# Kernel tuning notes

Measured on AMD Instinct MI355X. Metric: run time of the kernel, lower is better.

Reference implementation:

```python
import jax, jax.numpy as jnp
import numpy as np

B, C, H, W = 8, 64, 64, 64
CI = 32  # inter_channels = in_channels // 2
EPS = 1e-5


def conv1x1(x, w, b=None):
    # x: (b,c,h,w), w: (o,c) -> (b,o,h,w)
    y = jnp.einsum('bchw,oc->bohw', x, w)
    if b is not None:
        y = y + b[None, :, None, None]
    return y


def maxpool2x2(x):
    b, c, h, w = x.shape
    return x.reshape(b, c, h // 2, 2, w // 2, 2).max(axis=(3, 5))


def setup_inputs() -> dict:
    key = jax.random.key(0)
    ks = jax.random.split(key, 12)
    s = 0.05
    return {
        'x': jax.random.normal(ks[0], (B, C, H, W), jnp.float32),
        'theta_w': jax.random.normal(ks[1], (CI, C), jnp.float32) * s,
        'theta_b': jax.random.normal(ks[2], (CI,), jnp.float32) * s,
        'phi_w': jax.random.normal(ks[3], (CI, C), jnp.float32) * s,
        'phi_b': jax.random.normal(ks[4], (CI,), jnp.float32) * s,
        'psi_w': jax.random.normal(ks[5], (CI, C), jnp.float32) * s,
        'psi_b': jax.random.normal(ks[6], (CI,), jnp.float32) * s,
        'cp_w': jax.random.normal(ks[7], (2 * CI,), jnp.float32) * s,  # concat_project 1x1, no bias
        'W_w': jax.random.normal(ks[8], (C, CI + 1), jnp.float32) * s,
        'W_b': jax.random.normal(ks[9], (C,), jnp.float32) * s,
        'bn_gamma': jax.random.normal(ks[10], (C,), jnp.float32) * s + 1.0,
        'bn_beta': jax.random.normal(ks[11], (C,), jnp.float32) * s,
    }


def reference(x, theta_w, theta_b, phi_w, phi_b, psi_w, psi_b, cp_w, W_w, W_b, bn_gamma, bn_beta):
    b = x.shape[0]
    # psi / phi branches get 2x2 maxpool (sub_sample=True default)
    psi_x = maxpool2x2(conv1x1(x, psi_w, psi_b)).reshape(b, CI, -1)      # (b,ci,M)
    psi_x = psi_x.transpose(0, 2, 1)                                     # (b,M,ci)
    theta_x = conv1x1(x, theta_w, theta_b).reshape(b, CI, -1)            # (b,ci,N)
    phi_x = maxpool2x2(conv1x1(x, phi_w, phi_b)).reshape(b, CI, -1)      # (b,ci,M)
    # concat_project(cat[theta_i, phi_j]) + ReLU == relu(w1.theta_i + w2.phi_j)
    w1, w2 = cp_w[:CI], cp_w[CI:]
    a = jnp.einsum('bcn,c->bn', theta_x, w1)                             # (b,N)
    bb = jnp.einsum('bcm,c->bm', phi_x, w2)                              # (b,M)
    f = jax.nn.relu(a[:, :, None] + bb[:, None, :])                      # (b,N,M)
    M = f.shape[-1]
    f_div_C = f / float(M)
    y = jnp.matmul(f_div_C, psi_x)                                       # (b,N,ci)
    y = y.transpose(0, 2, 1).reshape(b, CI, H, W)
    # r_structure_type='zero' -> zero structure channel
    structure_feat = jnp.zeros((b, 1, H, W), y.dtype)
    y = jnp.concatenate([y, structure_feat], axis=1)                     # (b,ci+1,H,W)
    wy = conv1x1(y, W_w, W_b)                                            # (b,C,H,W)
    # BatchNorm2d, training-mode batch stats, biased variance
    mu = wy.mean(axis=(0, 2, 3), keepdims=True)
    var = wy.var(axis=(0, 2, 3), keepdims=True)
    wy = (wy - mu) * jax.lax.rsqrt(var + EPS)
    wy = wy * bn_gamma[None, :, None, None] + bn_beta[None, :, None, None]
    return wy + x
```

## Files before the change

kernel.cpp:

```cpp
#include <hip/hip_runtime.h>

#define OFF_A    0
#define OFF_BB   32768
#define OFF_RK   40960
#define OFF_U    57344
#define OFF_T1   581632
#define OFF_T2   1106432
#define OFF_KK   1631232
#define OFF_MP1  1664000
#define OFF_MP2  1664512
#define OFF_HC   1665024
#define OFF_HS   1673224
#define OFF_HS2  1681424
#define OFF_BAR  1689624

__device__ __forceinline__ void stg(float* p, float v) {
    __hip_atomic_store(p, v, __ATOMIC_RELAXED, __HIP_MEMORY_SCOPE_AGENT);
}
__device__ __forceinline__ float ldg1(const float* p) {
    return __hip_atomic_load(p, __ATOMIC_RELAXED, __HIP_MEMORY_SCOPE_AGENT);
}
__device__ __forceinline__ void stgi(int* p, int v) {
    __hip_atomic_store(p, v, __ATOMIC_RELAXED, __HIP_MEMORY_SCOPE_AGENT);
}
__device__ __forceinline__ int ldgi(const int* p) {
    return __hip_atomic_load(p, __ATOMIC_RELAXED, __HIP_MEMORY_SCOPE_AGENT);
}
__device__ __forceinline__ void stgu(unsigned* p, unsigned v) {
    __hip_atomic_store(p, v, __ATOMIC_RELAXED, __HIP_MEMORY_SCOPE_AGENT);
}
__device__ __forceinline__ unsigned ldgu(const unsigned* p) {
    return __hip_atomic_load(p, __ATOMIC_RELAXED, __HIP_MEMORY_SCOPE_AGENT);
}

__device__ __forceinline__ void gbarBatch(float* ws, int b, unsigned goal)
{
    __syncthreads();
    if (threadIdx.x == 0) {
        unsigned* ctr = (unsigned*)(ws + OFF_BAR) + ((b + 1) << 5);
        __hip_atomic_fetch_add(ctr, 1u, __ATOMIC_RELAXED,
                               __HIP_MEMORY_SCOPE_AGENT);
        while (ldgu(ctr) < goal) __builtin_amdgcn_s_sleep(2);
    }
    __syncthreads();
}

__global__ __launch_bounds__(1024) void kA(
    const float* __restrict__ x, const float* __restrict__ theta_w,
    const float* __restrict__ theta_b, const float* __restrict__ phi_w,
    const float* __restrict__ phi_b, const float* __restrict__ psi_w,
    const float* __restrict__ psi_b, const float* __restrict__ cp_w,
    const float* __restrict__ Ww, float* __restrict__ ws)
{
    __shared__ float sh[7396];
    const int tid = threadIdx.x;
    const int bid = blockIdx.x;
    const int b   = bid >> 5;
    const int sub = bid & 31;
    unsigned* bars = (unsigned*)(ws + OFF_BAR);

    {
        if (bid == 0 && tid == 0) {
            for (int i = 0; i < 8; ++i) stgu(&bars[(i + 1) << 5], 0u);
        }
        if (tid < 97) {
            int e = sub*97 + tid;
            if (e < 1025)      stg(&ws[OFF_HC  + b*1025 + e], 0.0f);
            else if (e < 2050) stg(&ws[OFF_HS  + b*1025 + e - 1025], 0.0f);
            else if (e < 3075) stg(&ws[OFF_HS2 + b*1025 + e - 2050], 0.0f);
        }
        float* sm   = sh;
        float* sth  = sh + 4160;
        float* spsi = sh + 4228;
        float* sWw  = sh + 5284;
        for (int e = tid; e < 2048; e += 1024) {
            int i = e >> 6, c = e & 63;
            sm[i*130 + 2*c]     = phi_w[e];
            sm[i*130 + 2*c + 1] = psi_w[e];
        }
        for (int e = tid; e < 2048; e += 1024)
            sWw[(e >> 5)*33 + (e & 31)] = Ww[(e >> 5)*33 + (e & 31)];
        if (tid < 64) {
            float s = 0;
            for (int i = 0; i < 32; ++i) s += cp_w[i]*theta_w[i*64 + tid];
            sth[tid] = s;
        } else if (tid == 64) {
            float s = 0;
            for (int i = 0; i < 32; ++i) s += cp_w[i]*theta_b[i];
            sth[64] = s;
        }
        __syncthreads();
        if (bid == 0 && tid == 0) {
            stgu(&bars[288], 0x5A5A5A5Au);
            stgu(&bars[289], 0xA5A5A5A5u);
        }
        int i = tid & 31;
        int mIdx = tid >> 5;
        int m = (sub << 5) + mIdx;
        int ph = m >> 5, pw = m & 31;
        const float* xb = x + b*262144 + ph*128 + pw*2;
        const float2* wrow = (const float2*)(sm + i*130);
        float tb = sth[64];
        float p0=0,p1=0,p2=0,p3=0,s0=0,s1=0,s2=0,s3=0;
        float a0=tb,a1=tb,a2=tb,a3=tb;
        #pragma unroll 8
        for (int c = 0; c < 64; ++c) {
            float2 xa = *(const float2*)(xb + c*4096);
            float2 xc = *(const float2*)(xb + c*4096 + 64);
            float2 w  = wrow[c];
            float st  = sth[c];
            p0 += xa.x*w.x; p1 += xa.y*w.x; p2 += xc.x*w.x; p3 += xc.y*w.x;
            s0 += xa.x*w.y; s1 += xa.y*w.y; s2 += xc.x*w.y; s3 += xc.y*w.y;
            a0 += xa.x*st;  a1 += xa.y*st;  a2 += xc.x*st;  a3 += xc.y*st;
        }
        float pv = fmaxf(fmaxf(p0,p1), fmaxf(p2,p3)) + phi_b[i];
        float sv = fmaxf(fmaxf(s0,s1), fmaxf(s2,s3)) + psi_b[i];
        spsi[mIdx*33 + i] = sv;
        float v = pv * cp_w[32 + i];
        v += __shfl_xor(v, 16, 32);
        v += __shfl_xor(v,  8, 32);
        v += __shfl_xor(v,  4, 32);
        v += __shfl_xor(v,  2, 32);
        v += __shfl_xor(v,  1, 32);
        if (i == 0) {
            stg(&ws[OFF_BB + (b<<10) + m], v);
            int nb = (b<<12) + ph*128 + pw*2;
            stg(&ws[OFF_A + nb],      a0);
            stg(&ws[OFF_A + nb + 1],  a1);
            stg(&ws[OFF_A + nb + 64], a2);
            stg(&ws[OFF_A + nb + 65], a3);
        }
        __syncthreads();
        #pragma unroll
        for (int rep = 0; rep < 2; ++rep) {
            int o  = (tid >> 5) + (rep << 5);
            int ml = tid & 31;
            const float* pr = &spsi[ml*33];
            const float* wr = &sWw[o*33];
            float u = 0;
            #pragma unroll
            for (int i2 = 0; i2 < 32; ++i2) u += pr[i2]*wr[i2];
            stg(&ws[OFF_U + (((b<<6) + o)<<10) + (sub<<5) + ml], u);
        }
    }
    __syncthreads();
    if (tid == 0) {
        while ((ldgu(&bars[288]) ^ ldgu(&bars[289])) != 0xFFFFFFFFu)
            __builtin_amdgcn_s_sleep(2);
        unsigned* ctr = bars + ((b + 1) << 5);
        __hip_atomic_fetch_add(ctr, 1u, __ATOMIC_RELAXED,
                               __HIP_MEMORY_SCOPE_AGENT);
        while (ldgu(ctr) < 32u) __builtin_amdgcn_s_sleep(2);
    }
    __syncthreads();

    {
        float* sb = sh;
        sb[tid] = ldg1(&ws[OFF_BB + (b<<10) + tid]);
        __syncthreads();
        {
            int ml = tid >> 5, jl = tid & 31;
            int m = (sub << 5) + ml;
            float vv = sb[m];
            int cnt = 0;
            for (int s = 0; s < 32; ++s) {
                int j = jl + (s << 5);
                float u = sb[j];
                cnt += (u > vv || (u == vv && j < m)) ? 1 : 0;
            }
            cnt += __shfl_xor(cnt,  1, 32);
            cnt += __shfl_xor(cnt,  2, 32);
            cnt += __shfl_xor(cnt,  4, 32);
            cnt += __shfl_xor(cnt,  8, 32);
            cnt += __shfl_xor(cnt, 16, 32);
            if (jl == 0)
                stgi(&((int*)ws)[OFF_RK + (b<<10) + m], cnt);
        }
        {
            int l = tid >> 3, jl = tid & 7;
            int n = (sub << 7) + l;
            float av = ldg1(&ws[OFF_A + (b<<12) + n]);
            float tt = -av;
            const float2* sb2 = (const float2*)sb;
            int cnt = 0;
            for (int s = 0; s < 64; ++s) {
                float2 u = sb2[jl + (s << 3)];
                cnt += (u.x > tt) ? 1 : 0;
                cnt += (u.y > tt) ? 1 : 0;
            }
            cnt += __shfl_xor(cnt, 1, 8);
            cnt += __shfl_xor(cnt, 2, 8);
            cnt += __shfl_xor(cnt, 4, 8);
            if (jl == 0) {
                stgi(&((int*)ws)[OFF_KK + (b<<12) + n], cnt);
                atomicAdd(&ws[OFF_HC + b*1025 + cnt], 1.0f);
                atomicAdd(&ws[OFF_HS + b*1025 + cnt], av);
                atomicAdd(&ws[OFF_HS2 + b*1025 + cnt], av*av);
            }
        }
    }
    gbarBatch(ws, b, 64u);

    {
        int obase = sub << 1;
        float* ssb  = sh;
        float* sU0  = sh + 1024;
        float* sU1  = sh + 2048;
        float* shc  = sh + 3072;
        float* shs  = sh + 4097;
        float* shs2 = sh + 5122;
        float* swp1 = sh + 6148;
        float* swp2 = sh + 6180;
        {
            float bbv = ldg1(&ws[OFF_BB + (b<<10) + tid]);
            int   rk  = ldgi(&((const int*)ws)[OFF_RK + (b<<10) + tid]);
            float u0  = ldg1(&ws[OFF_U + (((b<<6) + obase)<<10) + tid]);
            float u1  = ldg1(&ws[OFF_U + (((b<<6) + obase + 1)<<10) + tid]);
            ssb[rk] = bbv;
            sU0[rk] = u0;
            sU1[rk] = u1;
            shc[tid]  = ldg1(&ws[OFF_HC  + b*1025 + tid]);
            shs[tid]  = ldg1(&ws[OFF_HS  + b*1025 + tid]);
            shs2[tid] = ldg1(&ws[OFF_HS2 + b*1025 + tid]);
            if (tid == 0) {
                shc[1024]  = ldg1(&ws[OFF_HC  + b*1025 + 1024]);
                shs[1024]  = ldg1(&ws[OFF_HS  + b*1025 + 1024]);
                shs2[1024] = ldg1(&ws[OFF_HS2 + b*1025 + 1024]);
            }
        }
        __syncthreads();
        int ch = tid >> 1, o2 = tid & 1;
        int o  = obase + o2;
        int wv = tid >> 6, chl = (tid & 63) >> 1;
        const float* sU = sh + 1024 + (o2 << 10);
        float p[2], sp[2];
        float s1 = 0, s2 = 0;
        #pragma unroll
        for (int jl = 0; jl < 2; ++jl) {
            int jj = (ch<<1) + jl;
            float v = sU[jj];
            p[jl] = v;
            sp[jl] = ssb[jj]*v;
            s1 += v; s2 += sp[jl];
        }
        float own1 = s1, own2 = s2;
        #pragma unroll
        for (int d = 1; d < 32; d <<= 1) {
            float u1 = __shfl_up(s1, d<<1, 64);
            float u2 = __shfl_up(s2, d<<1, 64);
            if (chl >= d) { s1 += u1; s2 += u2; }
        }
        if (chl == 31) { swp1[(wv<<1)+o2] = s1; swp2[(wv<<1)+o2] = s2; }
        __syncthreads();
        float off1 = 0, off2 = 0;
        for (int w = 0; w < 16; ++w) {
            if (w < wv) { off1 += swp1[(w<<1)+o2]; off2 += swp2[(w<<1)+o2]; }
        }
        float run1 = off1 + s1 - own1;
        float run2 = off2 + s2 - own2;
        float* T1 = ws + OFF_T1 + b*65600 + o;
        float* T2 = ws + OFF_T2 + b*65600 + o;
        if (ch == 0) { stg(&T1[0], 0.0f); stg(&T2[0], 0.0f); }
        const float inv = 1.0f/1024.0f;
        float m1 = 0, m2 = 0;
        #pragma unroll
        for (int jl = 0; jl < 2; ++jl) {
            int k = (ch<<1) + jl + 1;
            run1 += p[jl]; run2 += sp[jl];
            float t1 = run1*inv, t2 = run2*inv;
            stg(&T1[k<<6], t1);
            stg(&T2[k<<6], t2);
            float c = shc[k], sa_ = shs[k], sa2 = shs2[k];
            m1 += sa_*t1 + c*t2;
            m2 += (sa2*t1 + 2.0f*sa_*t2)*t1 + c*t2*t2;
        }
        m1 += __shfl_xor(m1,  2, 64); m2 += __shfl_xor(m2,  2, 64);
        m1 += __shfl_xor(m1,  4, 64); m2 += __shfl_xor(m2,  4, 64);
        m1 += __shfl_xor(m1,  8, 64); m2 += __shfl_xor(m2,  8, 64);
        m1 += __shfl_xor(m1, 16, 64); m2 += __shfl_xor(m2, 16, 64);
        m1 += __shfl_xor(m1, 32, 64); m2 += __shfl_xor(m2, 32, 64);
        __syncthreads();
        if (chl == 0) { swp1[(wv<<1)+o2] = m1; swp2[(wv<<1)+o2] = m2; }
        __syncthreads();
        if (tid < 2) {
            float a1 = 0, a2 = 0;
            for (int w = 0; w < 16; ++w) {
                a1 += swp1[(w<<1)+tid]; a2 += swp2[(w<<1)+tid];
            }
            stg(&ws[OFF_MP1 + (b<<6) + obase + tid], a1);
            stg(&ws[OFF_MP2 + (b<<6) + obase + tid], a2);
        }
    }
}

__global__ __launch_bounds__(1024) void kB(
    const float* __restrict__ x, const float* __restrict__ Wb,
    const float* __restrict__ gamma, const float* __restrict__ beta,
    const float* __restrict__ ws, float* __restrict__ out)
{
    __shared__ float tile[64*129];
    __shared__ float sa[128];
    __shared__ int   sk[128];
    __shared__ float sA[64];
    __shared__ float sD[64];
    const int tid = threadIdx.x;
    const int b   = blockIdx.x >> 5;
    const int n0  = (blockIdx.x & 31) << 7;
    if (tid < 128) {
        sa[tid] = ws[OFF_A + (b<<12) + n0 + tid];
        sk[tid] = ((const int*)ws)[OFF_KK + (b<<12) + n0 + tid];
    }
    if (tid < 64) {
        const float Ninv = 1.0f/32768.0f;
        float m1s = 0, m2s = 0;
        #pragma unroll
        for (int b3 = 0; b3 < 8; ++b3) {
            m1s += ws[OFF_MP1 + (b3<<6) + tid];
            m2s += ws[OFF_MP2 + (b3<<6) + tid];
        }
        float m1 = m1s * Ninv;
        float m2 = m2s * Ninv;
        float wb = Wb[tid];
        float mu  = m1 + wb;
        float E2  = m2 + 2.0f*wb*m1 + wb*wb;
        float var = E2 - mu*mu;
        float A = gamma[tid] * rsqrtf(var + 1e-5f);
        sA[tid] = A;
        sD[tid] = beta[tid] + A*(wb - mu);
    }
    __syncthreads();
    const float* T1 = ws + OFF_T1 + b*65600;
    const float* T2 = ws + OFF_T2 + b*65600;
    {
        int o = tid & 63, ng = tid >> 6;
        float Ao = sA[o], Do = sD[o];
        #pragma unroll
        for (int j = 0; j < 8; ++j) {
            int n = (ng << 3) + j;
            int k = sk[n];
            float a = sa[n];
            float t1 = T1[(k<<6) + o];
            float t2 = T2[(k<<6) + o];
            tile[o*129 + n] = Ao*(a*t1 + t2) + Do;
        }
    }
    __syncthreads();
    {
        int n = tid & 127, og = tid >> 7;
        #pragma unroll
        for (int j = 0; j < 8; ++j) {
            int o = (og << 3) + j;
            int idx = ((b<<6) + o)*4096 + n0 + n;
            out[idx] = tile[o*129 + n] + x[idx];
        }
    }
}

extern "C" void kernel_launch(void* const* d_in, const int* in_sizes, int n_in,
                              void* d_out, int out_size, void* d_ws, size_t ws_size,
                              hipStream_t stream)
{
    const float* x       = (const float*)d_in[0];
    const float* theta_w = (const float*)d_in[1];
    const float* theta_b = (const float*)d_in[2];
    const float* phi_w   = (const float*)d_in[3];
    const float* phi_b   = (const float*)d_in[4];
    const float* psi_w   = (const float*)d_in[5];
    const float* psi_b   = (const float*)d_in[6];
    const float* cp_w    = (const float*)d_in[7];
    const float* Ww      = (const float*)d_in[8];
    const float* Wb      = (const float*)d_in[9];
    const float* gamma   = (const float*)d_in[10];
    const float* beta    = (const float*)d_in[11];
    float* ws  = (float*)d_ws;
    float* out = (float*)d_out;

    kA<<<256, 1024, 0, stream>>>(x, theta_w, theta_b, phi_w, phi_b,
                                 psi_w, psi_b, cp_w, Ww, ws);
    kB<<<256, 1024, 0, stream>>>(x, Wb, gamma, beta, ws, out);
}
```

Baseline: 126.2 us.

## Split persistent kernel with in-kernel grid barriers into four separate launches

Replaces the single kernel that used software spin barriers (per-batch atomic counters and a magic-number flag) with three kernels separated by launch boundaries. The global stores and loads become plain accesses instead of relaxed atomics. The T1/T2 tables are transposed to a per-channel contiguous layout (o*1025+k). The final kernel uses smaller 64-column tiles with 512 blocks of 512 threads. This removes spin-wait and atomic-access overhead but adds two extra launch gaps.

```diff
diff --git a/kernel.cpp b/kernel.cpp
--- a/kernel.cpp
+++ b/kernel.cpp
@@ -12,305 +12,253 @@
 #define OFF_HC   1665024
 #define OFF_HS   1673224
 #define OFF_HS2  1681424
-#define OFF_BAR  1689624
-
-__device__ __forceinline__ void stg(float* p, float v) {
-    __hip_atomic_store(p, v, __ATOMIC_RELAXED, __HIP_MEMORY_SCOPE_AGENT);
-}
-__device__ __forceinline__ float ldg1(const float* p) {
-    return __hip_atomic_load(p, __ATOMIC_RELAXED, __HIP_MEMORY_SCOPE_AGENT);
-}
-__device__ __forceinline__ void stgi(int* p, int v) {
-    __hip_atomic_store(p, v, __ATOMIC_RELAXED, __HIP_MEMORY_SCOPE_AGENT);
-}
-__device__ __forceinline__ int ldgi(const int* p) {
-    return __hip_atomic_load(p, __ATOMIC_RELAXED, __HIP_MEMORY_SCOPE_AGENT);
-}
-__device__ __forceinline__ void stgu(unsigned* p, unsigned v) {
-    __hip_atomic_store(p, v, __ATOMIC_RELAXED, __HIP_MEMORY_SCOPE_AGENT);
-}
-__device__ __forceinline__ unsigned ldgu(const unsigned* p) {
-    return __hip_atomic_load(p, __ATOMIC_RELAXED, __HIP_MEMORY_SCOPE_AGENT);
-}
-
-__device__ __forceinline__ void gbarBatch(float* ws, int b, unsigned goal)
-{
-    __syncthreads();
-    if (threadIdx.x == 0) {
-        unsigned* ctr = (unsigned*)(ws + OFF_BAR) + ((b + 1) << 5);
-        __hip_atomic_fetch_add(ctr, 1u, __ATOMIC_RELAXED,
-                               __HIP_MEMORY_SCOPE_AGENT);
-        while (ldgu(ctr) < goal) __builtin_amdgcn_s_sleep(2);
-    }
-    __syncthreads();
-}
-
-__global__ __launch_bounds__(1024) void kA(
+
+__global__ __launch_bounds__(1024) void k1(
     const float* __restrict__ x, const float* __restrict__ theta_w,
     const float* __restrict__ theta_b, const float* __restrict__ phi_w,
     const float* __restrict__ phi_b, const float* __restrict__ psi_w,
     const float* __restrict__ psi_b, const float* __restrict__ cp_w,
     const float* __restrict__ Ww, float* __restrict__ ws)
 {
-    __shared__ float sh[7396];
+    __shared__ float sm[4160];
+    __shared__ float sth[68];
+    __shared__ float spsi[32*33];
+    __shared__ float sWw[64*33];
     const int tid = threadIdx.x;
     const int bid = blockIdx.x;
     const int b   = bid >> 5;
     const int sub = bid & 31;
-    unsigned* bars = (unsigned*)(ws + OFF_BAR);
-
-    {
-        if (bid == 0 && tid == 0) {
-            for (int i = 0; i < 8; ++i) stgu(&bars[(i + 1) << 5], 0u);
-        }
-        if (tid < 97) {
-            int e = sub*97 + tid;
-            if (e < 1025)      stg(&ws[OFF_HC  + b*1025 + e], 0.0f);
-            else if (e < 2050) stg(&ws[OFF_HS  + b*1025 + e - 1025], 0.0f);
-            else if (e < 3075) stg(&ws[OFF_HS2 + b*1025 + e - 2050], 0.0f);
-        }
-        float* sm   = sh;
-        float* sth  = sh + 4160;
-        float* spsi = sh + 4228;
-        float* sWw  = sh + 5284;
-        for (int e = tid; e < 2048; e += 1024) {
-            int i = e >> 6, c = e & 63;
-            sm[i*130 + 2*c]     = phi_w[e];
-            sm[i*130 + 2*c + 1] = psi_w[e];
-        }
-        for (int e = tid; e < 2048; e += 1024)
-            sWw[(e >> 5)*33 + (e & 31)] = Ww[(e >> 5)*33 + (e & 31)];
-        if (tid < 64) {
-            float s = 0;
-            for (int i = 0; i < 32; ++i) s += cp_w[i]*theta_w[i*64 + tid];
-            sth[tid] = s;
-        } else if (tid == 64) {
-            float s = 0;
-            for (int i = 0; i < 32; ++i) s += cp_w[i]*theta_b[i];
-            sth[64] = s;
-        }
-        __syncthreads();
-        if (bid == 0 && tid == 0) {
-            stgu(&bars[288], 0x5A5A5A5Au);
-            stgu(&bars[289], 0xA5A5A5A5u);
-        }
-        int i = tid & 31;
-        int mIdx = tid >> 5;
-        int m = (sub << 5) + mIdx;
-        int ph = m >> 5, pw = m & 31;
-        const float* xb = x + b*262144 + ph*128 + pw*2;
-        const float2* wrow = (const float2*)(sm + i*130);
-        float tb = sth[64];
-        float p0=0,p1=0,p2=0,p3=0,s0=0,s1=0,s2=0,s3=0;
-        float a0=tb,a1=tb,a2=tb,a3=tb;
-        #pragma unroll 8
-        for (int c = 0; c < 64; ++c) {
-            float2 xa = *(const float2*)(xb + c*4096);
-            float2 xc = *(const float2*)(xb + c*4096 + 64);
-            float2 w  = wrow[c];
-            float st  = sth[c];
-            p0 += xa.x*w.x; p1 += xa.y*w.x; p2 += xc.x*w.x; p3 += xc.y*w.x;
-            s0 += xa.x*w.y; s1 += xa.y*w.y; s2 += xc.x*w.y; s3 += xc.y*w.y;
-            a0 += xa.x*st;  a1 += xa.y*st;  a2 += xc.x*st;  a3 += xc.y*st;
-        }
-        float pv = fmaxf(fmaxf(p0,p1), fmaxf(p2,p3)) + phi_b[i];
-        float sv = fmaxf(fmaxf(s0,s1), fmaxf(s2,s3)) + psi_b[i];
-        spsi[mIdx*33 + i] = sv;
-        float v = pv * cp_w[32 + i];
-        v += __shfl_xor(v, 16, 32);
-        v += __shfl_xor(v,  8, 32);
-        v += __shfl_xor(v,  4, 32);
-        v += __shfl_xor(v,  2, 32);
-        v += __shfl_xor(v,  1, 32);
-        if (i == 0) {
-            stg(&ws[OFF_BB + (b<<10) + m], v);
-            int nb = (b<<12) + ph*128 + pw*2;
-            stg(&ws[OFF_A + nb],      a0);
-            stg(&ws[OFF_A + nb + 1],  a1);
-            stg(&ws[OFF_A + nb + 64], a2);
-            stg(&ws[OFF_A + nb + 65], a3);
-        }
-        __syncthreads();
+
+    if (tid < 97) {
+        int e = sub*97 + tid;
+        if (e < 1025)      ws[OFF_HC  + b*1025 + e] = 0.0f;
+        else if (e < 2050) ws[OFF_HS  + b*1025 + e - 1025] = 0.0f;
+        else if (e < 3075) ws[OFF_HS2 + b*1025 + e - 2050] = 0.0f;
+    }
+    for (int e = tid; e < 2048; e += 1024) {
+        int i = e >> 6, c = e & 63;
+        sm[i*130 + 2*c]     = phi_w[e];
+        sm[i*130 + 2*c + 1] = psi_w[e];
+    }
+    for (int e = tid; e < 2048; e += 1024)
+        sWw[(e >> 5)*33 + (e & 31)] = Ww[(e >> 5)*33 + (e & 31)];
+    if (tid < 64) {
+        float s = 0;
+        for (int i = 0; i < 32; ++i) s += cp_w[i]*theta_w[i*64 + tid];
+        sth[tid] = s;
+    } else if (tid == 64) {
+        float s = 0;
+        for (int i = 0; i < 32; ++i) s += cp_w[i]*theta_b[i];
+        sth[64] = s;
+    }
+    __syncthreads();
+    int i = tid & 31;
+    int mIdx = tid >> 5;
+    int m = (sub << 5) + mIdx;
+    int ph = m >> 5, pw = m & 31;
+    const float* xb = x + b*262144 + ph*128 + pw*2;
+    const float2* wrow = (const float2*)(sm + i*130);
+    float tb = sth[64];
+    float p0=0,p1=0,p2=0,p3=0,s0=0,s1=0,s2=0,s3=0;
+    float a0=tb,a1=tb,a2=tb,a3=tb;
+    #pragma unroll 8
+    for (int c = 0; c < 64; ++c) {
+        float2 xa = *(const float2*)(xb + c*4096);
+        float2 xc = *(const float2*)(xb + c*4096 + 64);
+        float2 w  = wrow[c];
+        float st  = sth[c];
+        p0 += xa.x*w.x; p1 += xa.y*w.x; p2 += xc.x*w.x; p3 += xc.y*w.x;
+        s0 += xa.x*w.y; s1 += xa.y*w.y; s2 += xc.x*w.y; s3 += xc.y*w.y;
+        a0 += xa.x*st;  a1 += xa.y*st;  a2 += xc.x*st;  a3 += xc.y*st;
+    }
+    float pv = fmaxf(fmaxf(p0,p1), fmaxf(p2,p3)) + phi_b[i];
+    float sv = fmaxf(fmaxf(s0,s1), fmaxf(s2,s3)) + psi_b[i];
+    spsi[mIdx*33 + i] = sv;
+    float v = pv * cp_w[32 + i];
+    v += __shfl_xor(v, 16, 32);
+    v += __shfl_xor(v,  8, 32);
+    v += __shfl_xor(v,  4, 32);
+    v += __shfl_xor(v,  2, 32);
+    v += __shfl_xor(v,  1, 32);
+    if (i == 0) {
+        ws[OFF_BB + (b<<10) + m] = v;
+        int nb = (b<<12) + ph*128 + pw*2;
+        ws[OFF_A + nb]      = a0;
+        ws[OFF_A + nb + 1]  = a1;
+        ws[OFF_A + nb + 64] = a2;
+        ws[OFF_A + nb + 65] = a3;
+    }
+    __syncthreads();
+    #pragma unroll
+    for (int rep = 0; rep < 2; ++rep) {
+        int o  = (tid >> 5) + (rep << 5);
+        int ml = tid & 31;
+        const float* pr = &spsi[ml*33];
+        const float* wr = &sWw[o*33];
+        float u = 0;
         #pragma unroll
-        for (int rep = 0; rep < 2; ++rep) {
-            int o  = (tid >> 5) + (rep << 5);
-            int ml = tid & 31;
-            const float* pr = &spsi[ml*33];
-            const float* wr = &sWw[o*33];
-            float u = 0;
-            #pragma unroll
-            for (int i2 = 0; i2 < 32; ++i2) u += pr[i2]*wr[i2];
-            stg(&ws[OFF_U + (((b<<6) + o)<<10) + (sub<<5) + ml], u);
-        }
-    }
-    __syncthreads();
-    if (tid == 0) {
-        while ((ldgu(&bars[288]) ^ ldgu(&bars[289])) != 0xFFFFFFFFu)
-            __builtin_amdgcn_s_sleep(2);
-        unsigned* ctr = bars + ((b + 1) << 5);
-        __hip_atomic_fetch_add(ctr, 1u, __ATOMIC_RELAXED,
-                               __HIP_MEMORY_SCOPE_AGENT);
-        while (ldgu(ctr) < 32u) __builtin_amdgcn_s_sleep(2);
-    }
-    __syncthreads();
-
-    {
-        float* sb = sh;
-        sb[tid] = ldg1(&ws[OFF_BB + (b<<10) + tid]);
-        __syncthreads();
-        {
-            int ml = tid >> 5, jl = tid & 31;
-            int m = (sub << 5) + ml;
-            float vv = sb[m];
-            int cnt = 0;
-            for (int s = 0; s < 32; ++s) {
-                int j = jl + (s << 5);
-                float u = sb[j];
-                cnt += (u > vv || (u == vv && j < m)) ? 1 : 0;
-            }
-            cnt += __shfl_xor(cnt,  1, 32);
-            cnt += __shfl_xor(cnt,  2, 32);
-            cnt += __shfl_xor(cnt,  4, 32);
-            cnt += __shfl_xor(cnt,  8, 32);
-            cnt += __shfl_xor(cnt, 16, 32);
-            if (jl == 0)
-                stgi(&((int*)ws)[OFF_RK + (b<<10) + m], cnt);
-        }
-        {
-            int l = tid >> 3, jl = tid & 7;
-            int n = (sub << 7) + l;
-            float av = ldg1(&ws[OFF_A + (b<<12) + n]);
-            float tt = -av;
-            const float2* sb2 = (const float2*)sb;
-            int cnt = 0;
-            for (int s = 0; s < 64; ++s) {
-                float2 u = sb2[jl + (s << 3)];
-                cnt += (u.x > tt) ? 1 : 0;
-                cnt += (u.y > tt) ? 1 : 0;
-            }
-            cnt += __shfl_xor(cnt, 1, 8);
-            cnt += __shfl_xor(cnt, 2, 8);
-            cnt += __shfl_xor(cnt, 4, 8);
-            if (jl == 0) {
-                stgi(&((int*)ws)[OFF_KK + (b<<12) + n], cnt);
-                atomicAdd(&ws[OFF_HC + b*1025 + cnt], 1.0f);
-                atomicAdd(&ws[OFF_HS + b*1025 + cnt], av);
-                atomicAdd(&ws[OFF_HS2 + b*1025 + cnt], av*av);
-            }
-        }
-    }
-    gbarBatch(ws, b, 64u);
-
-    {
-        int obase = sub << 1;
-        float* ssb  = sh;
-        float* sU0  = sh + 1024;
-        float* sU1  = sh + 2048;
-        float* shc  = sh + 3072;
-        float* shs  = sh + 4097;
-        float* shs2 = sh + 5122;
-        float* swp1 = sh + 6148;
-        float* swp2 = sh + 6180;
-        {
-            float bbv = ldg1(&ws[OFF_BB + (b<<10) + tid]);
-            int   rk  = ldgi(&((const int*)ws)[OFF_RK + (b<<10) + tid]);
-            float u0  = ldg1(&ws[OFF_U + (((b<<6) + obase)<<10) + tid]);
-            float u1  = ldg1(&ws[OFF_U + (((b<<6) + obase + 1)<<10) + tid]);
-            ssb[rk] = bbv;
-            sU0[rk] = u0;
-            sU1[rk] = u1;
-            shc[tid]  = ldg1(&ws[OFF_HC  + b*1025 + tid]);
-            shs[tid]  = ldg1(&ws[OFF_HS  + b*1025 + tid]);
-            shs2[tid] = ldg1(&ws[OFF_HS2 + b*1025 + tid]);
-            if (tid == 0) {
-                shc[1024]  = ldg1(&ws[OFF_HC  + b*1025 + 1024]);
-                shs[1024]  = ldg1(&ws[OFF_HS  + b*1025 + 1024]);
-                shs2[1024] = ldg1(&ws[OFF_HS2 + b*1025 + 1024]);
-            }
-        }
-        __syncthreads();
-        int ch = tid >> 1, o2 = tid & 1;
-        int o  = obase + o2;
-        int wv = tid >> 6, chl = (tid & 63) >> 1;
-        const float* sU = sh + 1024 + (o2 << 10);
-        float p[2], sp[2];
-        float s1 = 0, s2 = 0;
-        #pragma unroll
-        for (int jl = 0; jl < 2; ++jl) {
-            int jj = (ch<<1) + jl;
-            float v = sU[jj];
-            p[jl] = v;
-            sp[jl] = ssb[jj]*v;
-            s1 += v; s2 += sp[jl];
-        }
-        float own1 = s1, own2 = s2;
-        #pragma unroll
-        for (int d = 1; d < 32; d <<= 1) {
-            float u1 = __shfl_up(s1, d<<1, 64);
-            float u2 = __shfl_up(s2, d<<1, 64);
-            if (chl >= d) { s1 += u1; s2 += u2; }
-        }
-        if (chl == 31) { swp1[(wv<<1)+o2] = s1; swp2[(wv<<1)+o2] = s2; }
-        __syncthreads();
-        float off1 = 0, off2 = 0;
+        for (int i2 = 0; i2 < 32; ++i2) u += pr[i2]*wr[i2];
+        ws[OFF_U + (((b<<6) + o)<<10) + (sub<<5) + ml] = u;
+    }
+}
+
+__global__ __launch_bounds__(1024) void k2(float* __restrict__ ws)
+{
+    __shared__ float sb[1024];
+    const int tid = threadIdx.x;
+    const int b   = blockIdx.x >> 5;
+    const int sub = blockIdx.x & 31;
+    sb[tid] = ws[OFF_BB + (b<<10) + tid];
+    __syncthreads();
+    {
+        int ml = tid >> 5, jl = tid & 31;
+        int m = (sub << 5) + ml;
+        float vv = sb[m];
+        int cnt = 0;
+        for (int s = 0; s < 32; ++s) {
+            int j = jl + (s << 5);
+            float u = sb[j];
+            cnt += (u > vv || (u == vv && j < m)) ? 1 : 0;
+        }
+        cnt += __shfl_xor(cnt,  1, 32);
+        cnt += __shfl_xor(cnt,  2, 32);
+        cnt += __shfl_xor(cnt,  4, 32);
+        cnt += __shfl_xor(cnt,  8, 32);
+        cnt += __shfl_xor(cnt, 16, 32);
+        if (jl == 0)
+            ((int*)ws)[OFF_RK + (b<<10) + m] = cnt;
+    }
+    {
+        int l = tid >> 3, jl = tid & 7;
+        int n = (sub << 7) + l;
+        float av = ws[OFF_A + (b<<12) + n];
+        float tt = -av;
+        const float2* sb2 = (const float2*)sb;
+        int cnt = 0;
+        for (int s = 0; s < 64; ++s) {
+            float2 u = sb2[jl + (s << 3)];
+            cnt += (u.x > tt) ? 1 : 0;
+            cnt += (u.y > tt) ? 1 : 0;
+        }
+        cnt += __shfl_xor(cnt, 1, 8);
+        cnt += __shfl_xor(cnt, 2, 8);
+        cnt += __shfl_xor(cnt, 4, 8);
+        if (jl == 0) {
+            ((int*)ws)[OFF_KK + (b<<12) + n] = cnt;
+            atomicAdd(&ws[OFF_HC + b*1025 + cnt], 1.0f);
+            atomicAdd(&ws[OFF_HS + b*1025 + cnt], av);
+            atomicAdd(&ws[OFF_HS2 + b*1025 + cnt], av*av);
+        }
+    }
+}
+
+__global__ __launch_bounds__(1024) void k3(float* __restrict__ ws)
+{
+    __shared__ float ssb[1024];
+    __shared__ float sU0[1024];
+    __shared__ float sU1[1024];
+    __shared__ float shc[1025], shs[1025], shs2[1025];
+    __shared__ float swp1[32], swp2[32];
+    const int tid = threadIdx.x;
+    const int b   = blockIdx.x >> 5;
+    const int obase = (blockIdx.x & 31) << 1;
+    {
+        float bbv = ws[OFF_BB + (b<<10) + tid];
+        int   rk  = ((const int*)ws)[OFF_RK + (b<<10) + tid];
+        float u0  = ws[OFF_U + (((b<<6) + obase)<<10) + tid];
+        float u1  = ws[OFF_U + (((b<<6) + obase + 1)<<10) + tid];
+        ssb[rk] = bbv;
+        sU0[rk] = u0;
+        sU1[rk] = u1;
+        shc[tid]  = ws[OFF_HC  + b*1025 + tid];
+        shs[tid]  = ws[OFF_HS  + b*1025 + tid];
+        shs2[tid] = ws[OFF_HS2 + b*1025 + tid];
+        if (tid == 0) {
+            shc[1024]  = ws[OFF_HC  + b*1025 + 1024];
+            shs[1024]  = ws[OFF_HS  + b*1025 + 1024];
+            shs2[1024] = ws[OFF_HS2 + b*1025 + 1024];
+        }
+    }
+    __syncthreads();
+    int ch = tid >> 1, o2 = tid & 1;
+    int o  = obase + o2;
+    int wv = tid >> 6, chl = (tid & 63) >> 1;
+    const float* sU = o2 ? sU1 : sU0;
+    float p[2], sp[2];
+    float s1 = 0, s2 = 0;
+    #pragma unroll
+    for (int jl = 0; jl < 2; ++jl) {
+        int jj = (ch<<1) + jl;
+        float v = sU[jj];
+        p[jl] = v;
+        sp[jl] = ssb[jj]*v;
+        s1 += v; s2 += sp[jl];
+    }
+    float own1 = s1, own2 = s2;
+    #pragma unroll
+    for (int d = 1; d < 32; d <<= 1) {
+        float u1 = __shfl_up(s1, d<<1, 64);
+        float u2 = __shfl_up(s2, d<<1, 64);
+        if (chl >= d) { s1 += u1; s2 += u2; }
+    }
+    if (chl == 31) { swp1[(wv<<1)+o2] = s1; swp2[(wv<<1)+o2] = s2; }
+    __syncthreads();
+    float off1 = 0, off2 = 0;
+    for (int w = 0; w < 16; ++w) {
+        if (w < wv) { off1 += swp1[(w<<1)+o2]; off2 += swp2[(w<<1)+o2]; }
+    }
+    float run1 = off1 + s1 - own1;
+    float run2 = off2 + s2 - own2;
+    float* T1 = ws + OFF_T1 + (((b<<6) + o)*1025);
+    float* T2 = ws + OFF_T2 + (((b<<6) + o)*1025);
+    if (ch == 0) { T1[0] = 0.0f; T2[0] = 0.0f; }
+    const float inv = 1.0f/1024.0f;
+    float m1 = 0, m2 = 0;
+    #pragma unroll
+    for (int jl = 0; jl < 2; ++jl) {
+        int k = (ch<<1) + jl + 1;
+        run1 += p[jl]; run2 += sp[jl];
+        float t1 = run1*inv, t2 = run2*inv;
+        T1[k] = t1;
+        T2[k] = t2;
+        float c = shc[k], sa_ = shs[k], sa2 = shs2[k];
+        m1 += sa_*t1 + c*t2;
+        m2 += (sa2*t1 + 2.0f*sa_*t2)*t1 + c*t2*t2;
+    }
+    m1 += __shfl_xor(m1,  2, 64); m2 += __shfl_xor(m2,  2, 64);
+    m1 += __shfl_xor(m1,  4, 64); m2 += __shfl_xor(m2,  4, 64);
+    m1 += __shfl_xor(m1,  8, 64); m2 += __shfl_xor(m2,  8, 64);
+    m1 += __shfl_xor(m1, 16, 64); m2 += __shfl_xor(m2, 16, 64);
+    m1 += __shfl_xor(m1, 32, 64); m2 += __shfl_xor(m2, 32, 64);
+    __syncthreads();
+    if (chl == 0) { swp1[(wv<<1)+o2] = m1; swp2[(wv<<1)+o2] = m2; }
+    __syncthreads();
+    if (tid < 2) {
+        float a1 = 0, a2 = 0;
         for (int w = 0; w < 16; ++w) {
-            if (w < wv) { off1 += swp1[(w<<1)+o2]; off2 += swp2[(w<<1)+o2]; }
-        }
-        float run1 = off1 + s1 - own1;
-        float run2 = off2 + s2 - own2;
-        float* T1 = ws + OFF_T1 + b*65600 + o;
-        float* T2 = ws + OFF_T2 + b*65600 + o;
-        if (ch == 0) { stg(&T1[0], 0.0f); stg(&T2[0], 0.0f); }
-        const float inv = 1.0f/1024.0f;
-        float m1 = 0, m2 = 0;
-        #pragma unroll
-        for (int jl = 0; jl < 2; ++jl) {
-            int k = (ch<<1) + jl + 1;
-            run1 += p[jl]; run2 += sp[jl];
-            float t1 = run1*inv, t2 = run2*inv;
-            stg(&T1[k<<6], t1);
-            stg(&T2[k<<6], t2);
-            float c = shc[k], sa_ = shs[k], sa2 = shs2[k];
-            m1 += sa_*t1 + c*t2;
-            m2 += (sa2*t1 + 2.0f*sa_*t2)*t1 + c*t2*t2;
-        }
-        m1 += __shfl_xor(m1,  2, 64); m2 += __shfl_xor(m2,  2, 64);
-        m1 += __shfl_xor(m1,  4, 64); m2 += __shfl_xor(m2,  4, 64);
-        m1 += __shfl_xor(m1,  8, 64); m2 += __shfl_xor(m2,  8, 64);
-        m1 += __shfl_xor(m1, 16, 64); m2 += __shfl_xor(m2, 16, 64);
-        m1 += __shfl_xor(m1, 32, 64); m2 += __shfl_xor(m2, 32, 64);
-        __syncthreads();
-        if (chl == 0) { swp1[(wv<<1)+o2] = m1; swp2[(wv<<1)+o2] = m2; }
-        __syncthreads();
-        if (tid < 2) {
-            float a1 = 0, a2 = 0;
-            for (int w = 0; w < 16; ++w) {
-                a1 += swp1[(w<<1)+tid]; a2 += swp2[(w<<1)+tid];
-            }
-            stg(&ws[OFF_MP1 + (b<<6) + obase + tid], a1);
-            stg(&ws[OFF_MP2 + (b<<6) + obase + tid], a2);
-        }
-    }
-}
-
-__global__ __launch_bounds__(1024) void kB(
+            a1 += swp1[(w<<1)+tid]; a2 += swp2[(w<<1)+tid];
+        }
+        ws[OFF_MP1 + (b<<6) + obase + tid] = a1;
+        ws[OFF_MP2 + (b<<6) + obase + tid] = a2;
+    }
+}
+
+__global__ __launch_bounds__(512) void k4(
     const float* __restrict__ x, const float* __restrict__ Wb,
     const float* __restrict__ gamma, const float* __restrict__ beta,
     const float* __restrict__ ws, float* __restrict__ out)
 {
-    __shared__ float tile[64*129];
-    __shared__ float sa[128];
-    __shared__ int   sk[128];
+    __shared__ float tile[64*65];
+    __shared__ float sa[64];
+    __shared__ int   sk[64];
     __shared__ float sA[64];
     __shared__ float sD[64];
     const int tid = threadIdx.x;
-    const int b   = blockIdx.x >> 5;
-    const int n0  = (blockIdx.x & 31) << 7;
-    if (tid < 128) {
+    const int b   = blockIdx.x >> 6;
+    const int n0  = (blockIdx.x & 63) << 6;
+    if (tid < 64) {
         sa[tid] = ws[OFF_A + (b<<12) + n0 + tid];
         sk[tid] = ((const int*)ws)[OFF_KK + (b<<12) + n0 + tid];
-    }
-    if (tid < 64) {
         const float Ninv = 1.0f/32768.0f;
         float m1s = 0, m2s = 0;
         #pragma unroll
@@ -329,29 +277,29 @@
         sD[tid] = beta[tid] + A*(wb - mu);
     }
     __syncthreads();
-    const float* T1 = ws + OFF_T1 + b*65600;
-    const float* T2 = ws + OFF_T2 + b*65600;
+    const float* T1 = ws + OFF_T1 + ((b<<6)*1025);
+    const float* T2 = ws + OFF_T2 + ((b<<6)*1025);
     {
         int o = tid & 63, ng = tid >> 6;
         float Ao = sA[o], Do = sD[o];
+        const float* T1o = T1 + o*1025;
+        const float* T2o = T2 + o*1025;
         #pragma unroll
         for (int j = 0; j < 8; ++j) {
             int n = (ng << 3) + j;
             int k = sk[n];
             float a = sa[n];
-            float t1 = T1[(k<<6) + o];
-            float t2 = T2[(k<<6) + o];
-            tile[o*129 + n] = Ao*(a*t1 + t2) + Do;
-        }
-    }
-    __syncthreads();
-    {
-        int n = tid & 127, og = tid >> 7;
+            tile[o*65 + n] = Ao*(a*T1o[k] + T2o[k]) + Do;
+        }
+    }
+    __syncthreads();
+    {
+        int n = tid & 63, og = tid >> 6;
         #pragma unroll
         for (int j = 0; j < 8; ++j) {
             int o = (og << 3) + j;
             int idx = ((b<<6) + o)*4096 + n0 + n;
-            out[idx] = tile[o*129 + n] + x[idx];
+            out[idx] = tile[o*65 + n] + x[idx];
         }
     }
 }
@@ -375,7 +323,9 @@
     float* ws  = (float*)d_ws;
     float* out = (float*)d_out;
 
-    kA<<<256, 1024, 0, stream>>>(x, theta_w, theta_b, phi_w, phi_b,
+    k1<<<256, 1024, 0, stream>>>(x, theta_w, theta_b, phi_w, phi_b,
                                  psi_w, psi_b, cp_w, Ww, ws);
-    kB<<<256, 1024, 0, stream>>>(x, Wb, gamma, beta, ws, out);
-}
+    k2<<<256, 1024, 0, stream>>>(ws);
+    k3<<<256, 1024, 0, stream>>>(ws);
+    k4<<<512, 512, 0, stream>>>(x, Wb, gamma, beta, ws, out);
+}
```

Result: slower. 135.1 us (+7.0%).

## Transpose T tables to per-channel layout, cache theta projection in LDS, split kB finer

Applied to the files above, without the earlier changes.

The T1/T2 prefix tables are stored per output channel (o*1025+k) instead of k-major with stride 64, which changes the access pattern of both the writes in kA and the gathers in kB. Each block keeps its own slice of the theta projection in shared memory, so the rank-count phase no longer reads it back from global memory. Several relaxed atomic stores become plain stores. kB moves to 512 blocks of 512 threads with 64-column tiles. The plain stores drop the atomic-scope semantics, and the code relies on the custom barrier plus the kernel boundary for visibility of the data written before the barrier.

```diff
diff --git a/kernel.cpp b/kernel.cpp
--- a/kernel.cpp
+++ b/kernel.cpp
@@ -33,18 +33,6 @@
     return __hip_atomic_load(p, __ATOMIC_RELAXED, __HIP_MEMORY_SCOPE_AGENT);
 }
 
-__device__ __forceinline__ void gbarBatch(float* ws, int b, unsigned goal)
-{
-    __syncthreads();
-    if (threadIdx.x == 0) {
-        unsigned* ctr = (unsigned*)(ws + OFF_BAR) + ((b + 1) << 5);
-        __hip_atomic_fetch_add(ctr, 1u, __ATOMIC_RELAXED,
-                               __HIP_MEMORY_SCOPE_AGENT);
-        while (ldgu(ctr) < goal) __builtin_amdgcn_s_sleep(2);
-    }
-    __syncthreads();
-}
-
 __global__ __launch_bounds__(1024) void kA(
     const float* __restrict__ x, const float* __restrict__ theta_w,
     const float* __restrict__ theta_b, const float* __restrict__ phi_w,
@@ -52,12 +40,13 @@
     const float* __restrict__ psi_b, const float* __restrict__ cp_w,
     const float* __restrict__ Ww, float* __restrict__ ws)
 {
-    __shared__ float sh[7396];
+    __shared__ float sh[7524];
     const int tid = threadIdx.x;
     const int bid = blockIdx.x;
     const int b   = bid >> 5;
     const int sub = bid & 31;
     unsigned* bars = (unsigned*)(ws + OFF_BAR);
+    float* sA2 = sh + 7396;
 
     {
         if (bid == 0 && tid == 0) {
@@ -125,10 +114,15 @@
         if (i == 0) {
             stg(&ws[OFF_BB + (b<<10) + m], v);
             int nb = (b<<12) + ph*128 + pw*2;
-            stg(&ws[OFF_A + nb],      a0);
-            stg(&ws[OFF_A + nb + 1],  a1);
-            stg(&ws[OFF_A + nb + 64], a2);
-            stg(&ws[OFF_A + nb + 65], a3);
+            ws[OFF_A + nb]      = a0;
+            ws[OFF_A + nb + 1]  = a1;
+            ws[OFF_A + nb + 64] = a2;
+            ws[OFF_A + nb + 65] = a3;
+            int nl = pw*2;
+            sA2[nl]      = a0;
+            sA2[nl + 1]  = a1;
+            sA2[nl + 64] = a2;
+            sA2[nl + 65] = a3;
         }
         __syncthreads();
         #pragma unroll
@@ -179,7 +173,7 @@
         {
             int l = tid >> 3, jl = tid & 7;
             int n = (sub << 7) + l;
-            float av = ldg1(&ws[OFF_A + (b<<12) + n]);
+            float av = sA2[l];
             float tt = -av;
             const float2* sb2 = (const float2*)sb;
             int cnt = 0;
@@ -192,17 +186,24 @@
             cnt += __shfl_xor(cnt, 2, 8);
             cnt += __shfl_xor(cnt, 4, 8);
             if (jl == 0) {
-                stgi(&((int*)ws)[OFF_KK + (b<<12) + n], cnt);
+                ((int*)ws)[OFF_KK + (b<<12) + n] = cnt;
                 atomicAdd(&ws[OFF_HC + b*1025 + cnt], 1.0f);
                 atomicAdd(&ws[OFF_HS + b*1025 + cnt], av);
                 atomicAdd(&ws[OFF_HS2 + b*1025 + cnt], av*av);
             }
         }
     }
-    gbarBatch(ws, b, 64u);
-
-    {
-        int obase = sub << 1;
+    __syncthreads();
+    if (tid == 0) {
+        unsigned* ctr = bars + ((b + 1) << 5);
+        __hip_atomic_fetch_add(ctr, 1u, __ATOMIC_RELAXED,
+                               __HIP_MEMORY_SCOPE_AGENT);
+        while (ldgu(ctr) < 64u) __builtin_amdgcn_s_sleep(2);
+    }
+    __syncthreads();
+
+    {
+        const int obase = sub << 1;
         float* ssb  = sh;
         float* sU0  = sh + 1024;
         float* sU1  = sh + 2048;
@@ -232,7 +233,7 @@
         int ch = tid >> 1, o2 = tid & 1;
         int o  = obase + o2;
         int wv = tid >> 6, chl = (tid & 63) >> 1;
-        const float* sU = sh + 1024 + (o2 << 10);
+        const float* sU = o2 ? sU1 : sU0;
         float p[2], sp[2];
         float s1 = 0, s2 = 0;
         #pragma unroll
@@ -258,9 +259,9 @@
         }
         float run1 = off1 + s1 - own1;
         float run2 = off2 + s2 - own2;
-        float* T1 = ws + OFF_T1 + b*65600 + o;
-        float* T2 = ws + OFF_T2 + b*65600 + o;
-        if (ch == 0) { stg(&T1[0], 0.0f); stg(&T2[0], 0.0f); }
+        float* T1 = ws + OFF_T1 + (((b<<6) + o)*1025);
+        float* T2 = ws + OFF_T2 + (((b<<6) + o)*1025);
+        if (ch == 0) { T1[0] = 0.0f; T2[0] = 0.0f; }
         const float inv = 1.0f/1024.0f;
         float m1 = 0, m2 = 0;
         #pragma unroll
@@ -268,8 +269,8 @@
             int k = (ch<<1) + jl + 1;
             run1 += p[jl]; run2 += sp[jl];
             float t1 = run1*inv, t2 = run2*inv;
-            stg(&T1[k<<6], t1);
-            stg(&T2[k<<6], t2);
+            T1[k] = t1;
+            T2[k] = t2;
             float c = shc[k], sa_ = shs[k], sa2 = shs2[k];
             m1 += sa_*t1 + c*t2;
             m2 += (sa2*t1 + 2.0f*sa_*t2)*t1 + c*t2*t2;
@@ -287,30 +288,28 @@
             for (int w = 0; w < 16; ++w) {
                 a1 += swp1[(w<<1)+tid]; a2 += swp2[(w<<1)+tid];
             }
-            stg(&ws[OFF_MP1 + (b<<6) + obase + tid], a1);
-            stg(&ws[OFF_MP2 + (b<<6) + obase + tid], a2);
-        }
-    }
-}
-
-__global__ __launch_bounds__(1024) void kB(
+            ws[OFF_MP1 + (b<<6) + obase + tid] = a1;
+            ws[OFF_MP2 + (b<<6) + obase + tid] = a2;
+        }
+    }
+}
+
+__global__ __launch_bounds__(512) void kB(
     const float* __restrict__ x, const float* __restrict__ Wb,
     const float* __restrict__ gamma, const float* __restrict__ beta,
     const float* __restrict__ ws, float* __restrict__ out)
 {
-    __shared__ float tile[64*129];
-    __shared__ float sa[128];
-    __shared__ int   sk[128];
+    __shared__ float tile[64*65];
+    __shared__ float sa[64];
+    __shared__ int   sk[64];
     __shared__ float sA[64];
     __shared__ float sD[64];
     const int tid = threadIdx.x;
-    const int b   = blockIdx.x >> 5;
-    const int n0  = (blockIdx.x & 31) << 7;
-    if (tid < 128) {
+    const int b   = blockIdx.x >> 6;
+    const int n0  = (blockIdx.x & 63) << 6;
+    if (tid < 64) {
         sa[tid] = ws[OFF_A + (b<<12) + n0 + tid];
         sk[tid] = ((const int*)ws)[OFF_KK + (b<<12) + n0 + tid];
-    }
-    if (tid < 64) {
         const float Ninv = 1.0f/32768.0f;
         float m1s = 0, m2s = 0;
         #pragma unroll
@@ -329,29 +328,29 @@
         sD[tid] = beta[tid] + A*(wb - mu);
     }
     __syncthreads();
-    const float* T1 = ws + OFF_T1 + b*65600;
-    const float* T2 = ws + OFF_T2 + b*65600;
+    const float* T1 = ws + OFF_T1 + ((b<<6)*1025);
+    const float* T2 = ws + OFF_T2 + ((b<<6)*1025);
     {
         int o = tid & 63, ng = tid >> 6;
         float Ao = sA[o], Do = sD[o];
+        const float* T1o = T1 + o*1025;
+        const float* T2o = T2 + o*1025;
         #pragma unroll
         for (int j = 0; j < 8; ++j) {
             int n = (ng << 3) + j;
             int k = sk[n];
             float a = sa[n];
-            float t1 = T1[(k<<6) + o];
-            float t2 = T2[(k<<6) + o];
-            tile[o*129 + n] = Ao*(a*t1 + t2) + Do;
-        }
-    }
-    __syncthreads();
-    {
-        int n = tid & 127, og = tid >> 7;
+            tile[o*65 + n] = Ao*(a*T1o[k] + T2o[k]) + Do;
+        }
+    }
+    __syncthreads();
+    {
+        int n = tid & 63, og = tid >> 6;
         #pragma unroll
         for (int j = 0; j < 8; ++j) {
             int o = (og << 3) + j;
             int idx = ((b<<6) + o)*4096 + n0 + n;
-            out[idx] = tile[o*129 + n] + x[idx];
+            out[idx] = tile[o*65 + n] + x[idx];
         }
     }
 }
@@ -377,5 +376,5 @@
 
     kA<<<256, 1024, 0, stream>>>(x, theta_w, theta_b, phi_w, phi_b,
                                  psi_w, psi_b, cp_w, Ww, ws);
-    kB<<<256, 1024, 0, stream>>>(x, Wb, gamma, beta, ws, out);
-}
+    kB<<<512, 512, 0, stream>>>(x, Wb, gamma, beta, ws, out);
+}
```

After: 133.5 us. 1.06x slower.
